# Optimization experiments

Hardware: AMD Instinct MI355X
Metric: run time of the kernel (lower is better)

## Reference

```python
import jax, jax.numpy as jnp
import numpy as np

N_NODES = 50000
N_EDGES = 800000
IN_C, HID, OUT_C = 128, 128, 16
N_GRAPHS = 128


def setup_inputs() -> dict:
    key = jax.random.key(0)
    ks = jax.random.split(key, 8)
    x = jax.random.normal(ks[0], (N_NODES, IN_C), dtype=jnp.float32)
    edge_index = jax.random.randint(ks[1], (2, N_EDGES), 0, N_NODES, dtype=jnp.int64)
    batch = jnp.sort(jax.random.randint(ks[2], (N_NODES,), 0, N_GRAPHS, dtype=jnp.int64))
    s1 = 1.0 / np.sqrt(IN_C)
    s2 = 1.0 / np.sqrt(HID)
    W1 = jax.random.normal(ks[3], (IN_C, HID), dtype=jnp.float32) * s1
    b1 = jnp.zeros((HID,), dtype=jnp.float32)
    W2 = jax.random.normal(ks[4], (HID, HID), dtype=jnp.float32) * s2
    b2 = jnp.zeros((HID,), dtype=jnp.float32)
    Wfc = jax.random.normal(ks[5], (HID, OUT_C), dtype=jnp.float32) * s2
    bfc = jnp.zeros((OUT_C,), dtype=jnp.float32)
    return {"x": x, "edge_index": edge_index, "batch": batch,
            "W1": W1, "b1": b1, "W2": W2, "b2": b2, "Wfc": Wfc, "bfc": bfc}


def _gcn_conv(x, W, b, src, dst, deg_inv_sqrt, n_nodes):
    # linear transform first (PyG order), then normalized sparse aggregation
    h = x @ W  # [N, H]
    norm = deg_inv_sqrt[src] * deg_inv_sqrt[dst]  # [E+N] (self-loops appended)
    msgs = h[src] * norm[:, None]  # [E+N, H] dominant gather
    agg = jax.ops.segment_sum(msgs, dst, num_segments=n_nodes)
    return agg + b


def reference(x, edge_index, batch, W1, b1, W2, b2, Wfc, bfc):
    n = x.shape[0]
    loops = jnp.arange(n, dtype=edge_index.dtype)
    src = jnp.concatenate([edge_index[0], loops])
    dst = jnp.concatenate([edge_index[1], loops])
    # symmetric normalization with self-loops: deg computed on dst
    deg = jax.ops.segment_sum(jnp.ones_like(src, dtype=x.dtype), dst, num_segments=n)
    deg_inv_sqrt = jnp.where(deg > 0, jax.lax.rsqrt(jnp.maximum(deg, 1.0)), 0.0)

    h = jax.nn.relu(_gcn_conv(x, W1, b1, src, dst, deg_inv_sqrt, n))
    h = jax.nn.relu(_gcn_conv(h, W2, b2, src, dst, deg_inv_sqrt, n))

    # global mean pool over graph ids
    sums = jax.ops.segment_sum(h, batch, num_segments=N_GRAPHS)
    counts = jax.ops.segment_sum(jnp.ones((n,), dtype=h.dtype), batch, num_segments=N_GRAPHS)
    pooled = sums / jnp.maximum(counts, 1.0)[:, None]  # [G, H]

    logits = pooled @ Wfc + bfc  # [G, OUT_C]
    return jax.nn.log_softmax(logits, axis=1)
```

## Files before the change

kernel.cpp:

```cpp
#include <hip/hip_runtime.h>

#define N_NODES  50000
#define N_EDGES  800000
#define HID      128
#define OUT_C    16
#define N_GRAPHS 128
#define MAXDEG   64
#define NSLICE   6250
#define EPB      1024
#define AGB      3125
#define PAD      136

#define GRP      72
#define NGRP     97
#define GB0      6984

typedef __attribute__((ext_vector_type(8))) short bf16x8;
typedef __attribute__((ext_vector_type(4))) float f32x4;
typedef __attribute__((ext_vector_type(8))) unsigned short us8;
typedef __attribute__((ext_vector_type(4))) unsigned short us4;

__device__ __forceinline__ unsigned short f2bf(float f) {
  unsigned u = __float_as_uint(f);
  u += 0x7fffu + ((u >> 16) & 1u);
  return (unsigned short)(u >> 16);
}

__device__ __forceinline__ void gemm_compute_store(
    unsigned short* sA, const float* __restrict__ W,
    unsigned short* __restrict__ T, int base) {
  const int tid = threadIdx.x;
  const int lane = tid & 63;
  const int w = tid >> 6;
  const int l15 = lane & 15;
  const int quad = lane >> 4;
  __syncthreads();

  f32x4 acc[4][2];
#pragma unroll
  for (int nt = 0; nt < 4; ++nt)
#pragma unroll
    for (int c = 0; c < 2; ++c) acc[nt][c] = (f32x4)(0.f);

  const int ct0 = w * 2;
  const int ncol = ct0 * 16 + l15;
#pragma unroll
  for (int ks = 0; ks < 4; ++ks) {
    const int koff = ks * 32 + quad * 8;
    bf16x8 a[4], bfr[2];
#pragma unroll
    for (int c = 0; c < 2; ++c) {
      const float* wp = W + (size_t)koff * HID + ncol + c * 16;
#pragma unroll
      for (int j = 0; j < 8; ++j) bfr[c][j] = (short)f2bf(wp[(size_t)j * HID]);
    }
#pragma unroll
    for (int nt = 0; nt < 4; ++nt)
      a[nt] = *(const bf16x8*)(sA + (nt * 16 + l15) * PAD + koff);
#pragma unroll
    for (int nt = 0; nt < 4; ++nt)
#pragma unroll
      for (int c = 0; c < 2; ++c)
        acc[nt][c] = __builtin_amdgcn_mfma_f32_16x16x32_bf16(a[nt], bfr[c], acc[nt][c], 0, 0, 0);
  }
  __syncthreads();

#pragma unroll
  for (int nt = 0; nt < 4; ++nt)
#pragma unroll
    for (int c = 0; c < 2; ++c)
#pragma unroll
      for (int r = 0; r < 4; ++r)
        sA[(nt * 16 + quad * 4 + r) * PAD + (ct0 + c) * 16 + l15] = f2bf(acc[nt][c][r]);
  __syncthreads();
#pragma unroll
  for (int i = 0; i < 4; ++i) {
    int idx = tid + i * 256;
    int nrow = idx >> 4;
    int col = (idx & 15) * 8;
    int node = base + nrow;
    if (node < N_NODES)
      *(us8*)(T + (size_t)node * HID + col) = *(const us8*)(sA + nrow * PAD + col);
  }
}

__device__ __forceinline__ void stage_a_f32(unsigned short* sA,
                                            const float* __restrict__ H, int base) {
#pragma unroll
  for (int i = 0; i < 8; ++i) {
    int idx = threadIdx.x + i * 256;
    int nrow = idx >> 5;
    int c4 = (idx & 31) * 4;
    f32x4 v = (f32x4)(0.f);
    int node = base + nrow;
    if (node < N_NODES)
      v = __builtin_nontemporal_load((const f32x4*)(H + (size_t)node * HID + c4));
    us4 b;
    b.x = f2bf(v.x); b.y = f2bf(v.y); b.z = f2bf(v.z); b.w = f2bf(v.w);
    *(us4*)(sA + nrow * PAD + c4) = b;
  }
}

__global__ __launch_bounds__(256) void mega_kernel(
    const int* __restrict__ src, const int* __restrict__ dst,
    int* __restrict__ deg, unsigned short* __restrict__ ell,
    const int* __restrict__ batch, int* __restrict__ start,
    const float* __restrict__ x, const float* __restrict__ W1,
    unsigned short* __restrict__ T) {
  __shared__ unsigned short sA[64 * PAD];
  const int b = blockIdx.x;
  int fi = -1, gi = -1;
  if (b < GB0) {
    const int g = b / GRP, r = b % GRP;
    if (r < 64) fi = g * 64 + r;
    else        gi = g * 8 + (r - 64);
  } else {
    const int r = b - GB0;
    if (r < 48)      fi = NGRP * 64 + r;
    else if (r < 54) gi = NGRP * 8 + (r - 48);
  }
  if (fi >= 0) {
    const int slice = fi & 7;
    const int e0 = (fi >> 3) * EPB;
    const int e1 = min(e0 + EPB, N_EDGES);
    const unsigned lo = slice * NSLICE;
    for (int e = e0 + threadIdx.x; e < e1; e += 256) {
      int d = __builtin_nontemporal_load(dst + e);
      if ((unsigned)(d - lo) < (unsigned)NSLICE) {
        int p = atomicAdd(&deg[d], 1);
        if (p < MAXDEG) ell[(d << 6) + p] = (unsigned short)src[e];
      }
    }
  } else if (gi >= 0) {
    const int base = gi * 64;
    stage_a_f32(sA, x, base);
    gemm_compute_store(sA, W1, T, base);
  } else {
    int t = threadIdx.x;
    if (t <= N_GRAPHS) {
      int lo = 0, hi = N_NODES;
      while (lo < hi) {
        int mid = (lo + hi) >> 1;
        if (batch[mid] < t) lo = mid + 1; else hi = mid;
      }
      start[t] = lo;
    }
  }
}

__device__ __forceinline__ void agg_node_pack(
    int node, int lane, const unsigned int* __restrict__ Tb,
    const unsigned short* __restrict__ ell, const int* __restrict__ deg,
    unsigned int* __restrict__ ellw,
    float bx, float by, float& ox, float& oy) {
  int dn = deg[node];
  float dd = rsqrtf((float)dn + 1.0f);
  unsigned sv = Tb[(size_t)node * 64 + lane];
  float wself = dd * dd;
  float ax = __int_as_float(sv << 16) * wself;
  float ay = __int_as_float(sv & 0xffff0000u) * wself;
  int m = min(dn, MAXDEG);
  int s0 = node << 6;
  int sidx = 0; float wv = 0.f;
  if (lane < m) {
    sidx = (int)ell[s0 + lane];
    wv = rsqrtf((float)deg[sidx] + 1.0f) * dd;
    unsigned short hw = __builtin_bit_cast(unsigned short, (_Float16)wv);
    ellw[s0 + lane] = (unsigned)sidx | ((unsigned)hw << 16);
  }
  const int mt = (m + 7) & ~7;
  for (int j = 0; j < mt; j += 8) {
#pragma unroll
    for (int q = 0; q < 8; ++q) {
      int s = __builtin_amdgcn_readlane(sidx, j + q);
      float w = __int_as_float(__builtin_amdgcn_readlane(__float_as_int(wv), j + q));
      unsigned t = Tb[(size_t)s * 64 + lane];
      ax += w * __int_as_float(t << 16);
      ay += w * __int_as_float(t & 0xffff0000u);
    }
  }
  ox = fmaxf(ax + bx, 0.f);
  oy = fmaxf(ay + by, 0.f);
}

__global__ __launch_bounds__(1024) void agg_gemm_kernel(
    const unsigned int* __restrict__ Tb, const unsigned short* __restrict__ ell,
    const int* __restrict__ deg, const float* __restrict__ bias,
    const float* __restrict__ W, unsigned int* __restrict__ ellw,
    unsigned short* __restrict__ T2) {
  __shared__ unsigned short sA[16 * PAD];
  const int tid = threadIdx.x;
  const int lane = tid & 63;
  const int w = tid >> 6;
  const int l15 = lane & 15;
  const int quad = lane >> 4;
  const int base = blockIdx.x * 16;

  {
    float2 b = ((const float2*)bias)[lane];
    float ox, oy;
    agg_node_pack(base + w, lane, Tb, ell, deg, ellw, b.x, b.y, ox, oy);
    *(unsigned*)(sA + w * PAD + lane * 2) =
        (unsigned)f2bf(ox) | ((unsigned)f2bf(oy) << 16);
  }
  __syncthreads();

  f32x4 acc = (f32x4)(0.f);
  if (w < 8) {
    const int ncol = w * 16 + l15;
#pragma unroll
    for (int ks = 0; ks < 4; ++ks) {
      const int koff = ks * 32 + quad * 8;
      bf16x8 a = *(const bf16x8*)(sA + l15 * PAD + koff);
      bf16x8 bfr;
      const float* wp = W + (size_t)koff * HID + ncol;
#pragma unroll
      for (int j = 0; j < 8; ++j) bfr[j] = (short)f2bf(wp[(size_t)j * HID]);
      acc = __builtin_amdgcn_mfma_f32_16x16x32_bf16(a, bfr, acc, 0, 0, 0);
    }
  }
  __syncthreads();
  if (w < 8) {
#pragma unroll
    for (int r = 0; r < 4; ++r)
      sA[(quad * 4 + r) * PAD + w * 16 + l15] = f2bf(acc[r]);
  }
  __syncthreads();
  if (tid < 256) {
    int nrow = tid >> 4;
    int col = (tid & 15) * 8;
    *(us8*)(T2 + (size_t)(base + nrow) * HID + col) = *(const us8*)(sA + nrow * PAD + col);
  }
}

__global__ __launch_bounds__(256) void aggregate_kernel(
    const unsigned int* __restrict__ Tb, const unsigned int* __restrict__ ellw,
    const int* __restrict__ deg, const float* __restrict__ bias,
    unsigned int* __restrict__ Hb) {
  int wid = (blockIdx.x * 256 + threadIdx.x) >> 6;
  int lane = threadIdx.x & 63;
  int n0 = wid * 2;
  if (n0 >= N_NODES) return;
  int n1 = n0 + 1;
  float2 b = ((const float2*)bias)[lane];
  int d0 = deg[n0], d1 = deg[n1];
  float r0 = rsqrtf((float)d0 + 1.f), r1 = rsqrtf((float)d1 + 1.f);
  unsigned sv0 = Tb[(size_t)n0 * 64 + lane];
  unsigned sv1 = Tb[(size_t)n1 * 64 + lane];
  float ax0 = __int_as_float(sv0 << 16) * (r0 * r0);
  float ay0 = __int_as_float(sv0 & 0xffff0000u) * (r0 * r0);
  float ax1 = __int_as_float(sv1 << 16) * (r1 * r1);
  float ay1 = __int_as_float(sv1 & 0xffff0000u) * (r1 * r1);
  int m0 = min(d0, MAXDEG), m1 = min(d1, MAXDEG);
  unsigned pw0 = 0, pw1 = 0;
  if (lane < m0) pw0 = ellw[(n0 << 6) + lane];
  if (lane < m1) pw1 = ellw[(n1 << 6) + lane];
  const int mt = (max(m0, m1) + 7) & ~7;
  for (int j = 0; j < mt; j += 8) {
#pragma unroll
    for (int q = 0; q < 8; ++q) {
      unsigned v0 = (unsigned)__builtin_amdgcn_readlane((int)pw0, j + q);
      unsigned v1 = (unsigned)__builtin_amdgcn_readlane((int)pw1, j + q);
      unsigned t0 = Tb[(size_t)(v0 & 0xffffu) * 64 + lane];
      unsigned t1 = Tb[(size_t)(v1 & 0xffffu) * 64 + lane];
      float w0 = (float)__builtin_bit_cast(_Float16, (unsigned short)(v0 >> 16));
      float w1 = (float)__builtin_bit_cast(_Float16, (unsigned short)(v1 >> 16));
      ax0 += w0 * __int_as_float(t0 << 16);
      ay0 += w0 * __int_as_float(t0 & 0xffff0000u);
      ax1 += w1 * __int_as_float(t1 << 16);
      ay1 += w1 * __int_as_float(t1 & 0xffff0000u);
    }
  }
  Hb[(size_t)n0 * 64 + lane] =
      (unsigned)f2bf(fmaxf(ax0 + b.x, 0.f)) |
      ((unsigned)f2bf(fmaxf(ay0 + b.y, 0.f)) << 16);
  Hb[(size_t)n1 * 64 + lane] =
      (unsigned)f2bf(fmaxf(ax1 + b.x, 0.f)) |
      ((unsigned)f2bf(fmaxf(ay1 + b.y, 0.f)) << 16);
}

__global__ __launch_bounds__(256) void pool_partial_kernel(
    const unsigned int* __restrict__ Hb, const int* __restrict__ start,
    float* __restrict__ pooled) {
  __shared__ float2 red[4][64];
  int g = blockIdx.x >> 2;
  int chunk = blockIdx.x & 3;
  int n0 = start[g], n1 = start[g + 1];
  int lane = threadIdx.x & 63, w = threadIdx.x >> 6;
  float ax = 0.f, ay = 0.f;
  for (int n = n0 + chunk * 4 + w; n < n1; n += 16) {
    unsigned h = Hb[(size_t)n * 64 + lane];
    ax += __int_as_float(h << 16);
    ay += __int_as_float(h & 0xffff0000u);
  }
  red[w][lane] = make_float2(ax, ay);
  __syncthreads();
  if (threadIdx.x < 64) {
    float2 a = red[0][lane], b = red[1][lane], c = red[2][lane], d = red[3][lane];
    atomicAdd(&pooled[g * HID + lane * 2],     a.x + b.x + c.x + d.x);
    atomicAdd(&pooled[g * HID + lane * 2 + 1], a.y + b.y + c.y + d.y);
  }
}

__global__ __launch_bounds__(64) void head_kernel(
    const float* __restrict__ pooled, const int* __restrict__ start,
    const float* __restrict__ Wfc, const float* __restrict__ bfc,
    float* __restrict__ out) {
  int g = blockIdx.x;
  int lane = threadIdx.x;
  int o = lane & 15;
  float inv = 1.0f / fmaxf((float)(start[g + 1] - start[g]), 1.0f);
  float part = 0.f;
  for (int k = (lane >> 4); k < HID; k += 4)
    part += pooled[g * HID + k] * inv * Wfc[k * OUT_C + o];
  part += __shfl_xor(part, 16);
  part += __shfl_xor(part, 32);
  float logit = part + bfc[o];
  float m = logit;
#pragma unroll
  for (int d = 8; d >= 1; d >>= 1) m = fmaxf(m, __shfl_xor(m, d, 16));
  float e = __expf(logit - m);
  float s = e;
#pragma unroll
  for (int d = 8; d >= 1; d >>= 1) s += __shfl_xor(s, d, 16);
  float r = logit - m - __logf(s);
  if (lane < 16) out[g * OUT_C + o] = r;
}

extern "C" void kernel_launch(void* const* d_in, const int* in_sizes, int n_in,
                              void* d_out, int out_size, void* d_ws, size_t ws_size,
                              hipStream_t stream) {
  const float* x    = (const float*)d_in[0];
  const int*   ei   = (const int*)d_in[1];
  const int*   batch= (const int*)d_in[2];
  const float* W1   = (const float*)d_in[3];
  const float* b1   = (const float*)d_in[4];
  const float* W2   = (const float*)d_in[5];
  const float* b2   = (const float*)d_in[6];
  const float* Wfc  = (const float*)d_in[7];
  const float* bfc  = (const float*)d_in[8];
  float* out = (float*)d_out;
  const int* src = ei;
  const int* dst = ei + N_EDGES;

  char* p = (char*)d_ws;
  auto alloc = [&](size_t bytes) { char* r = p; p += (bytes + 255) & ~255ull; return r; };
  int*   degI   = (int*)alloc((size_t)N_NODES * 4);
  float* pooled = (float*)alloc((size_t)N_GRAPHS * HID * 4);
  int*   start  = (int*)alloc((N_GRAPHS + 1) * 4);
  unsigned short* ell = (unsigned short*)alloc((size_t)N_NODES * MAXDEG * 2);
  unsigned int*   ellw= (unsigned int*)alloc((size_t)N_NODES * MAXDEG * 4);
  unsigned short* T   = (unsigned short*)alloc((size_t)N_NODES * HID * 2);
  unsigned short* T2  = (unsigned short*)alloc((size_t)N_NODES * HID * 2);
  unsigned short* Hb  = (unsigned short*)alloc((size_t)N_NODES * HID * 2);

  hipMemsetAsync(degI, 0, ((size_t)N_NODES * 4 + 255 & ~255ull) +
                          (size_t)N_GRAPHS * HID * 4, stream);

  int agg_blocks = (N_NODES / 2 * 64 + 255) / 256;

  mega_kernel<<<GB0 + 55, 256, 0, stream>>>(src, dst, degI, ell,
                                            batch, start, x, W1, T);
  agg_gemm_kernel<<<AGB, 1024, 0, stream>>>((const unsigned int*)T, ell, degI,
                                            b1, W2, ellw, T2);
  aggregate_kernel<<<agg_blocks, 256, 0, stream>>>((const unsigned int*)T2, ellw, degI, b2,
                                                   (unsigned int*)Hb);
  pool_partial_kernel<<<N_GRAPHS * 4, 256, 0, stream>>>((const unsigned int*)Hb, start,
                                                        pooled);
  head_kernel<<<N_GRAPHS, 64, 0, stream>>>(pooled, start, Wfc, bfc, out);
}
```

Baseline: 222.0 us.

## Aggregate two nodes per wave in fused agg-GEMM and use all 16 waves for MFMA

```diff
diff --git a/kernel.cpp b/kernel.cpp
--- a/kernel.cpp
+++ b/kernel.cpp
@@ -8,7 +8,7 @@
 #define MAXDEG   64
 #define NSLICE   6250
 #define EPB      1024
-#define AGB      3125
+#define NAGB     1563
 #define PAD      136
 
 #define GRP      72
@@ -148,39 +148,54 @@
   }
 }
 
-__device__ __forceinline__ void agg_node_pack(
-    int node, int lane, const unsigned int* __restrict__ Tb,
+__device__ __forceinline__ void agg_node_pack2(
+    int n0, int n1, int lane, const unsigned int* __restrict__ Tb,
     const unsigned short* __restrict__ ell, const int* __restrict__ deg,
-    unsigned int* __restrict__ ellw,
-    float bx, float by, float& ox, float& oy) {
-  int dn = deg[node];
-  float dd = rsqrtf((float)dn + 1.0f);
-  unsigned sv = Tb[(size_t)node * 64 + lane];
-  float wself = dd * dd;
-  float ax = __int_as_float(sv << 16) * wself;
-  float ay = __int_as_float(sv & 0xffff0000u) * wself;
-  int m = min(dn, MAXDEG);
-  int s0 = node << 6;
-  int sidx = 0; float wv = 0.f;
-  if (lane < m) {
-    sidx = (int)ell[s0 + lane];
-    wv = rsqrtf((float)deg[sidx] + 1.0f) * dd;
-    unsigned short hw = __builtin_bit_cast(unsigned short, (_Float16)wv);
-    ellw[s0 + lane] = (unsigned)sidx | ((unsigned)hw << 16);
-  }
-  const int mt = (m + 7) & ~7;
+    unsigned int* __restrict__ ellw, float bx, float by,
+    float& ox0, float& oy0, float& ox1, float& oy1) {
+  int d0 = deg[n0], d1 = deg[n1];
+  float dd0 = rsqrtf((float)d0 + 1.0f), dd1 = rsqrtf((float)d1 + 1.0f);
+  unsigned sv0 = Tb[(size_t)n0 * 64 + lane];
+  unsigned sv1 = Tb[(size_t)n1 * 64 + lane];
+  float ax0 = __int_as_float(sv0 << 16) * (dd0 * dd0);
+  float ay0 = __int_as_float(sv0 & 0xffff0000u) * (dd0 * dd0);
+  float ax1 = __int_as_float(sv1 << 16) * (dd1 * dd1);
+  float ay1 = __int_as_float(sv1 & 0xffff0000u) * (dd1 * dd1);
+  int m0 = min(d0, MAXDEG), m1 = min(d1, MAXDEG);
+  int sidx0 = 0, sidx1 = 0;
+  float wv0 = 0.f, wv1 = 0.f;
+  if (lane < m0) {
+    sidx0 = (int)ell[(n0 << 6) + lane];
+    wv0 = rsqrtf((float)deg[sidx0] + 1.0f) * dd0;
+    unsigned short hw = __builtin_bit_cast(unsigned short, (_Float16)wv0);
+    ellw[(n0 << 6) + lane] = (unsigned)sidx0 | ((unsigned)hw << 16);
+  }
+  if (lane < m1) {
+    sidx1 = (int)ell[(n1 << 6) + lane];
+    wv1 = rsqrtf((float)deg[sidx1] + 1.0f) * dd1;
+    unsigned short hw = __builtin_bit_cast(unsigned short, (_Float16)wv1);
+    ellw[(n1 << 6) + lane] = (unsigned)sidx1 | ((unsigned)hw << 16);
+  }
+  const int mt = (max(m0, m1) + 7) & ~7;
   for (int j = 0; j < mt; j += 8) {
 #pragma unroll
     for (int q = 0; q < 8; ++q) {
-      int s = __builtin_amdgcn_readlane(sidx, j + q);
-      float w = __int_as_float(__builtin_amdgcn_readlane(__float_as_int(wv), j + q));
-      unsigned t = Tb[(size_t)s * 64 + lane];
-      ax += w * __int_as_float(t << 16);
-      ay += w * __int_as_float(t & 0xffff0000u);
-    }
-  }
-  ox = fmaxf(ax + bx, 0.f);
-  oy = fmaxf(ay + by, 0.f);
+      int s0 = __builtin_amdgcn_readlane(sidx0, j + q);
+      int s1 = __builtin_amdgcn_readlane(sidx1, j + q);
+      float w0 = __int_as_float(__builtin_amdgcn_readlane(__float_as_int(wv0), j + q));
+      float w1 = __int_as_float(__builtin_amdgcn_readlane(__float_as_int(wv1), j + q));
+      unsigned t0 = Tb[(size_t)s0 * 64 + lane];
+      unsigned t1 = Tb[(size_t)s1 * 64 + lane];
+      ax0 += w0 * __int_as_float(t0 << 16);
+      ay0 += w0 * __int_as_float(t0 & 0xffff0000u);
+      ax1 += w1 * __int_as_float(t1 << 16);
+      ay1 += w1 * __int_as_float(t1 & 0xffff0000u);
+    }
+  }
+  ox0 = fmaxf(ax0 + bx, 0.f);
+  oy0 = fmaxf(ay0 + by, 0.f);
+  ox1 = fmaxf(ax1 + bx, 0.f);
+  oy1 = fmaxf(ay1 + by, 0.f);
 }
 
 __global__ __launch_bounds__(1024) void agg_gemm_kernel(
@@ -188,48 +203,52 @@
     const int* __restrict__ deg, const float* __restrict__ bias,
     const float* __restrict__ W, unsigned int* __restrict__ ellw,
     unsigned short* __restrict__ T2) {
-  __shared__ unsigned short sA[16 * PAD];
+  __shared__ unsigned short sA[32 * PAD];
   const int tid = threadIdx.x;
   const int lane = tid & 63;
   const int w = tid >> 6;
   const int l15 = lane & 15;
   const int quad = lane >> 4;
-  const int base = blockIdx.x * 16;
+  const int base = blockIdx.x * 32;
 
   {
     float2 b = ((const float2*)bias)[lane];
-    float ox, oy;
-    agg_node_pack(base + w, lane, Tb, ell, deg, ellw, b.x, b.y, ox, oy);
-    *(unsigned*)(sA + w * PAD + lane * 2) =
-        (unsigned)f2bf(ox) | ((unsigned)f2bf(oy) << 16);
-  }
-  __syncthreads();
-
+    int n0 = min(base + 2 * w,     N_NODES - 1);
+    int n1 = min(base + 2 * w + 1, N_NODES - 1);
+    float ox0, oy0, ox1, oy1;
+    agg_node_pack2(n0, n1, lane, Tb, ell, deg, ellw, b.x, b.y, ox0, oy0, ox1, oy1);
+    *(unsigned*)(sA + (2 * w) * PAD + lane * 2) =
+        (unsigned)f2bf(ox0) | ((unsigned)f2bf(oy0) << 16);
+    *(unsigned*)(sA + (2 * w + 1) * PAD + lane * 2) =
+        (unsigned)f2bf(ox1) | ((unsigned)f2bf(oy1) << 16);
+  }
+  __syncthreads();
+
+  const int rt = w >> 3;
+  const int ct = w & 7;
+  const int ncol = ct * 16 + l15;
   f32x4 acc = (f32x4)(0.f);
-  if (w < 8) {
-    const int ncol = w * 16 + l15;
-#pragma unroll
-    for (int ks = 0; ks < 4; ++ks) {
-      const int koff = ks * 32 + quad * 8;
-      bf16x8 a = *(const bf16x8*)(sA + l15 * PAD + koff);
-      bf16x8 bfr;
-      const float* wp = W + (size_t)koff * HID + ncol;
-#pragma unroll
-      for (int j = 0; j < 8; ++j) bfr[j] = (short)f2bf(wp[(size_t)j * HID]);
-      acc = __builtin_amdgcn_mfma_f32_16x16x32_bf16(a, bfr, acc, 0, 0, 0);
-    }
-  }
-  __syncthreads();
-  if (w < 8) {
-#pragma unroll
-    for (int r = 0; r < 4; ++r)
-      sA[(quad * 4 + r) * PAD + w * 16 + l15] = f2bf(acc[r]);
-  }
-  __syncthreads();
-  if (tid < 256) {
+#pragma unroll
+  for (int ks = 0; ks < 4; ++ks) {
+    const int koff = ks * 32 + quad * 8;
+    bf16x8 a = *(const bf16x8*)(sA + (rt * 16 + l15) * PAD + koff);
+    bf16x8 bfr;
+    const float* wp = W + (size_t)koff * HID + ncol;
+#pragma unroll
+    for (int j = 0; j < 8; ++j) bfr[j] = (short)f2bf(wp[(size_t)j * HID]);
+    acc = __builtin_amdgcn_mfma_f32_16x16x32_bf16(a, bfr, acc, 0, 0, 0);
+  }
+  __syncthreads();
+#pragma unroll
+  for (int r = 0; r < 4; ++r)
+    sA[(rt * 16 + quad * 4 + r) * PAD + ct * 16 + l15] = f2bf(acc[r]);
+  __syncthreads();
+  if (tid < 512) {
     int nrow = tid >> 4;
     int col = (tid & 15) * 8;
-    *(us8*)(T2 + (size_t)(base + nrow) * HID + col) = *(const us8*)(sA + nrow * PAD + col);
+    int node = base + nrow;
+    if (node < N_NODES)
+      *(us8*)(T2 + (size_t)node * HID + col) = *(const us8*)(sA + nrow * PAD + col);
   }
 }
 
@@ -361,8 +380,8 @@
 
   mega_kernel<<<GB0 + 55, 256, 0, stream>>>(src, dst, degI, ell,
                                             batch, start, x, W1, T);
-  agg_gemm_kernel<<<AGB, 1024, 0, stream>>>((const unsigned int*)T, ell, degI,
-                                            b1, W2, ellw, T2);
+  agg_gemm_kernel<<<NAGB, 1024, 0, stream>>>((const unsigned int*)T, ell, degI,
+                                             b1, W2, ellw, T2);
   aggregate_kernel<<<agg_blocks, 256, 0, stream>>>((const unsigned int*)T2, ellw, degI, b2,
                                                    (unsigned int*)Hb);
   pool_partial_kernel<<<N_GRAPHS * 4, 256, 0, stream>>>((const unsigned int*)Hb, start,
```

Result: no change. 223.3 us (+0.6%).

## Factor GCN normalization into pre-scaled features and drop per-edge weight array

Applied to the files above, without the earlier changes.

```diff
diff --git a/kernel.cpp b/kernel.cpp
--- a/kernel.cpp
+++ b/kernel.cpp
@@ -10,6 +10,8 @@
 #define EPB      1024
 #define AGB      3125
 #define PAD      136
+#define ZROW     N_NODES
+#define SCALEB   12501
 
 #define GRP      72
 #define NGRP     97
@@ -148,46 +150,52 @@
   }
 }
 
-__device__ __forceinline__ void agg_node_pack(
+__global__ __launch_bounds__(256) void scale_kernel(
+    unsigned int* __restrict__ Tb, unsigned int* __restrict__ T2b,
+    const int* __restrict__ deg) {
+  int idx = blockIdx.x * 256 + threadIdx.x;
+  if (idx < 64) T2b[(size_t)ZROW * 64 + idx] = 0u;
+  if (idx < N_NODES * 64) {
+    int node = idx >> 6;
+    float dd = rsqrtf((float)deg[node] + 1.0f);
+    unsigned v = Tb[idx];
+    float xx = __int_as_float(v << 16) * dd;
+    float yy = __int_as_float(v & 0xffff0000u) * dd;
+    Tb[idx] = (unsigned)f2bf(xx) | ((unsigned)f2bf(yy) << 16);
+  } else if (idx < N_NODES * 64 + 64) {
+    Tb[idx] = 0u;
+  }
+}
+
+__device__ __forceinline__ void agg_node_sum(
     int node, int lane, const unsigned int* __restrict__ Tb,
     const unsigned short* __restrict__ ell, const int* __restrict__ deg,
-    unsigned int* __restrict__ ellw,
     float bx, float by, float& ox, float& oy) {
   int dn = deg[node];
   float dd = rsqrtf((float)dn + 1.0f);
   unsigned sv = Tb[(size_t)node * 64 + lane];
-  float wself = dd * dd;
-  float ax = __int_as_float(sv << 16) * wself;
-  float ay = __int_as_float(sv & 0xffff0000u) * wself;
+  float ax = __int_as_float(sv << 16);
+  float ay = __int_as_float(sv & 0xffff0000u);
   int m = min(dn, MAXDEG);
-  int s0 = node << 6;
-  int sidx = 0; float wv = 0.f;
-  if (lane < m) {
-    sidx = (int)ell[s0 + lane];
-    wv = rsqrtf((float)deg[sidx] + 1.0f) * dd;
-    unsigned short hw = __builtin_bit_cast(unsigned short, (_Float16)wv);
-    ellw[s0 + lane] = (unsigned)sidx | ((unsigned)hw << 16);
-  }
+  int sidx = (lane < m) ? (int)ell[(node << 6) + lane] : ZROW;
   const int mt = (m + 7) & ~7;
   for (int j = 0; j < mt; j += 8) {
 #pragma unroll
     for (int q = 0; q < 8; ++q) {
       int s = __builtin_amdgcn_readlane(sidx, j + q);
-      float w = __int_as_float(__builtin_amdgcn_readlane(__float_as_int(wv), j + q));
       unsigned t = Tb[(size_t)s * 64 + lane];
-      ax += w * __int_as_float(t << 16);
-      ay += w * __int_as_float(t & 0xffff0000u);
-    }
-  }
-  ox = fmaxf(ax + bx, 0.f);
-  oy = fmaxf(ay + by, 0.f);
+      ax += __int_as_float(t << 16);
+      ay += __int_as_float(t & 0xffff0000u);
+    }
+  }
+  ox = fmaxf(dd * ax + bx, 0.f);
+  oy = fmaxf(dd * ay + by, 0.f);
 }
 
 __global__ __launch_bounds__(1024) void agg_gemm_kernel(
     const unsigned int* __restrict__ Tb, const unsigned short* __restrict__ ell,
     const int* __restrict__ deg, const float* __restrict__ bias,
-    const float* __restrict__ W, unsigned int* __restrict__ ellw,
-    unsigned short* __restrict__ T2) {
+    const float* __restrict__ W, unsigned short* __restrict__ T2) {
   __shared__ unsigned short sA[16 * PAD];
   const int tid = threadIdx.x;
   const int lane = tid & 63;
@@ -199,7 +207,7 @@
   {
     float2 b = ((const float2*)bias)[lane];
     float ox, oy;
-    agg_node_pack(base + w, lane, Tb, ell, deg, ellw, b.x, b.y, ox, oy);
+    agg_node_sum(base + w, lane, Tb, ell, deg, b.x, b.y, ox, oy);
     *(unsigned*)(sA + w * PAD + lane * 2) =
         (unsigned)f2bf(ox) | ((unsigned)f2bf(oy) << 16);
   }
@@ -222,8 +230,10 @@
   __syncthreads();
   if (w < 8) {
 #pragma unroll
-    for (int r = 0; r < 4; ++r)
-      sA[(quad * 4 + r) * PAD + w * 16 + l15] = f2bf(acc[r]);
+    for (int r = 0; r < 4; ++r) {
+      float dd2 = rsqrtf((float)deg[base + quad * 4 + r] + 1.0f);
+      sA[(quad * 4 + r) * PAD + w * 16 + l15] = f2bf(acc[r] * dd2);
+    }
   }
   __syncthreads();
   if (tid < 256) {
@@ -234,7 +244,7 @@
 }
 
 __global__ __launch_bounds__(256) void aggregate_kernel(
-    const unsigned int* __restrict__ Tb, const unsigned int* __restrict__ ellw,
+    const unsigned int* __restrict__ Tb, const unsigned short* __restrict__ ell,
     const int* __restrict__ deg, const float* __restrict__ bias,
     unsigned int* __restrict__ Hb) {
   int wid = (blockIdx.x * 256 + threadIdx.x) >> 6;
@@ -247,36 +257,33 @@
   float r0 = rsqrtf((float)d0 + 1.f), r1 = rsqrtf((float)d1 + 1.f);
   unsigned sv0 = Tb[(size_t)n0 * 64 + lane];
   unsigned sv1 = Tb[(size_t)n1 * 64 + lane];
-  float ax0 = __int_as_float(sv0 << 16) * (r0 * r0);
-  float ay0 = __int_as_float(sv0 & 0xffff0000u) * (r0 * r0);
-  float ax1 = __int_as_float(sv1 << 16) * (r1 * r1);
-  float ay1 = __int_as_float(sv1 & 0xffff0000u) * (r1 * r1);
+  float ax0 = __int_as_float(sv0 << 16);
+  float ay0 = __int_as_float(sv0 & 0xffff0000u);
+  float ax1 = __int_as_float(sv1 << 16);
+  float ay1 = __int_as_float(sv1 & 0xffff0000u);
   int m0 = min(d0, MAXDEG), m1 = min(d1, MAXDEG);
-  unsigned pw0 = 0, pw1 = 0;
-  if (lane < m0) pw0 = ellw[(n0 << 6) + lane];
-  if (lane < m1) pw1 = ellw[(n1 << 6) + lane];
+  int sidx0 = (lane < m0) ? (int)ell[(n0 << 6) + lane] : ZROW;
+  int sidx1 = (lane < m1) ? (int)ell[(n1 << 6) + lane] : ZROW;
   const int mt = (max(m0, m1) + 7) & ~7;
   for (int j = 0; j < mt; j += 8) {
 #pragma unroll
     for (int q = 0; q < 8; ++q) {
-      unsigned v0 = (unsigned)__builtin_amdgcn_readlane((int)pw0, j + q);
-      unsigned v1 = (unsigned)__builtin_amdgcn_readlane((int)pw1, j + q);
-      unsigned t0 = Tb[(size_t)(v0 & 0xffffu) * 64 + lane];
-      unsigned t1 = Tb[(size_t)(v1 & 0xffffu) * 64 + lane];
-      float w0 = (float)__builtin_bit_cast(_Float16, (unsigned short)(v0 >> 16));
-      float w1 = (float)__builtin_bit_cast(_Float16, (unsigned short)(v1 >> 16));
-      ax0 += w0 * __int_as_float(t0 << 16);
-      ay0 += w0 * __int_as_float(t0 & 0xffff0000u);
-      ax1 += w1 * __int_as_float(t1 << 16);
-      ay1 += w1 * __int_as_float(t1 & 0xffff0000u);
+      int s0 = __builtin_amdgcn_readlane(sidx0, j + q);
+      int s1 = __builtin_amdgcn_readlane(sidx1, j + q);
+      unsigned t0 = Tb[(size_t)s0 * 64 + lane];
+      unsigned t1 = Tb[(size_t)s1 * 64 + lane];
+      ax0 += __int_as_float(t0 << 16);
+      ay0 += __int_as_float(t0 & 0xffff0000u);
+      ax1 += __int_as_float(t1 << 16);
+      ay1 += __int_as_float(t1 & 0xffff0000u);
     }
   }
   Hb[(size_t)n0 * 64 + lane] =
-      (unsigned)f2bf(fmaxf(ax0 + b.x, 0.f)) |
-      ((unsigned)f2bf(fmaxf(ay0 + b.y, 0.f)) << 16);
+      (unsigned)f2bf(fmaxf(r0 * ax0 + b.x, 0.f)) |
+      ((unsigned)f2bf(fmaxf(r0 * ay0 + b.y, 0.f)) << 16);
   Hb[(size_t)n1 * 64 + lane] =
-      (unsigned)f2bf(fmaxf(ax1 + b.x, 0.f)) |
-      ((unsigned)f2bf(fmaxf(ay1 + b.y, 0.f)) << 16);
+      (unsigned)f2bf(fmaxf(r1 * ax1 + b.x, 0.f)) |
+      ((unsigned)f2bf(fmaxf(r1 * ay1 + b.y, 0.f)) << 16);
 }
 
 __global__ __launch_bounds__(256) void pool_partial_kernel(
@@ -349,9 +356,8 @@
   float* pooled = (float*)alloc((size_t)N_GRAPHS * HID * 4);
   int*   start  = (int*)alloc((N_GRAPHS + 1) * 4);
   unsigned short* ell = (unsigned short*)alloc((size_t)N_NODES * MAXDEG * 2);
-  unsigned int*   ellw= (unsigned int*)alloc((size_t)N_NODES * MAXDEG * 4);
-  unsigned short* T   = (unsigned short*)alloc((size_t)N_NODES * HID * 2);
-  unsigned short* T2  = (unsigned short*)alloc((size_t)N_NODES * HID * 2);
+  unsigned short* T   = (unsigned short*)alloc((size_t)(N_NODES + 1) * HID * 2);
+  unsigned short* T2  = (unsigned short*)alloc((size_t)(N_NODES + 1) * HID * 2);
   unsigned short* Hb  = (unsigned short*)alloc((size_t)N_NODES * HID * 2);
 
   hipMemsetAsync(degI, 0, ((size_t)N_NODES * 4 + 255 & ~255ull) +
@@ -361,9 +367,10 @@
 
   mega_kernel<<<GB0 + 55, 256, 0, stream>>>(src, dst, degI, ell,
                                             batch, start, x, W1, T);
+  scale_kernel<<<SCALEB, 256, 0, stream>>>((unsigned int*)T, (unsigned int*)T2, degI);
   agg_gemm_kernel<<<AGB, 1024, 0, stream>>>((const unsigned int*)T, ell, degI,
-                                            b1, W2, ellw, T2);
-  aggregate_kernel<<<agg_blocks, 256, 0, stream>>>((const unsigned int*)T2, ellw, degI, b2,
+                                            b1, W2, T2);
+  aggregate_kernel<<<agg_blocks, 256, 0, stream>>>((const unsigned int*)T2, ell, degI, b2,
                                                    (unsigned int*)Hb);
   pool_partial_kernel<<<N_GRAPHS * 4, 256, 0, stream>>>((const unsigned int*)Hb, start,
                                                         pooled);
```

After: 228.1 us. 1.03x slower.
